# Kernel tuning notes

Measured on AMD Instinct MI355X. Metric: run time of the kernel, lower is better.

## Reference

```python
import jax, jax.numpy as jnp
import numpy as np

EPS = 1e-7
R = 3  # routing iterations


def conv(x, k, b, stride):
    y = jax.lax.conv_general_dilated(x, k, (stride, stride), 'VALID',
                                     dimension_numbers=('NHWC', 'HWIO', 'NHWC'))
    return y + b


def squash(s):
    n = jnp.linalg.norm(s, axis=-1, keepdims=True)
    return (n * n) / (1.0 + n * n) * s / (n + EPS)


def setup_inputs() -> dict:
    key = jax.random.key(0)
    ks = jax.random.split(key, 12)
    B = 256

    def g(k, shape, scale=0.05):
        return jax.random.normal(k, shape, dtype=jnp.float32) * scale

    return dict(
        x=jax.random.normal(ks[0], (B, 40, 40, 1), dtype=jnp.float32),
        y=jax.random.randint(ks[1], (B,), 0, 10),
        conv1_k=g(ks[2], (5, 5, 1, 64)),   conv1_b=jnp.zeros((64,), jnp.float32),
        conv2_k=g(ks[3], (9, 9, 64, 128)), conv2_b=jnp.zeros((128,), jnp.float32),
        conv3_k=g(ks[4], (9, 9, 128, 256)), conv3_b=jnp.zeros((256,), jnp.float32),
        prim_k=g(ks[5], (9, 9, 256, 256)), prim_b=jnp.zeros((256,), jnp.float32),
        w=g(ks[6], (1152, 10, 16, 8)),
        d1_w=g(ks[7], (160, 1024)),  d1_b=jnp.zeros((1024,), jnp.float32),
        d2_w=g(ks[8], (1024, 2048)), d2_b=jnp.zeros((2048,), jnp.float32),
        d3_w=g(ks[9], (2048, 1600)), d3_b=jnp.zeros((1600,), jnp.float32),
    )


def reference(x, y, conv1_k, conv1_b, conv2_k, conv2_b, conv3_k, conv3_b,
              prim_k, prim_b, w, d1_w, d1_b, d2_w, d2_b, d3_w, d3_b):
    # conv stack: 40 -> 36 -> 28 -> 20 -> 6 (primary caps, stride 2, linear)
    h = jax.nn.relu(conv(x, conv1_k, conv1_b, 1))
    h = jax.nn.relu(conv(h, conv2_k, conv2_b, 1))
    h = jax.nn.relu(conv(h, conv3_k, conv3_b, 1))
    h = conv(h, prim_k, prim_b, 2)                      # [B,6,6,256]
    B = h.shape[0]
    u = h.reshape(B, 1152, 8)                           # 1152 primary capsules of dim 8

    # pose predictions: u_hat[b,i,j,k] = sum_v w[i,j,k,v] * u[b,i,v]
    u_hat = jnp.einsum('ijkv,biv->bijk', w, u)          # [B,1152,10,16]

    # dynamic routing by agreement
    b_logit = jnp.zeros((B, 1152, 10), dtype=u_hat.dtype)
    for _ in range(R):
        c = jax.nn.softmax(b_logit, axis=2)[..., None]          # [B,1152,10,1]
        s = jnp.sum(c * u_hat, axis=1, keepdims=True)           # [B,1,10,16]
        v = squash(s)                                           # [B,1,10,16]
        b_logit = b_logit + jnp.sum(u_hat * v, axis=-1)         # agreement

    # masking by true label and reconstruction
    yh = jax.nn.one_hot(y, 10, dtype=v.dtype)                   # [B,10]
    v_masked = yh[:, None, :, None] * v                         # [B,1,10,16]
    v_flat = v_masked.reshape(B, 10 * 16)
    r1 = jax.nn.relu(v_flat @ d1_w + d1_b)
    r2 = jax.nn.relu(r1 @ d2_w + d2_b)
    recon = jax.nn.sigmoid(r2 @ d3_w + d3_b)                    # [B,1600]
    return (v, recon)
```

## Files before the change

kernel.cpp:

```cpp
#include <hip/hip_runtime.h>
#include <hip/hip_bf16.h>

typedef _Float16 f16;
typedef __attribute__((ext_vector_type(8))) _Float16 f16x8;
typedef __attribute__((ext_vector_type(4))) float f32x4;

__device__ __forceinline__ void gload_lds16(const void* g, void* l) {
  __builtin_amdgcn_global_load_lds((const __attribute__((address_space(1))) void*)g,
                                   (__attribute__((address_space(3))) void*)l, 16, 0, 0);
}

template<int CIN, int COUT>
__global__ __launch_bounds__(256) void wtrans_kernel(const float* __restrict__ src,
                                                     f16* __restrict__ dst) {
  constexpr int KT = 81 * CIN;
  __shared__ float tile[64][65];
  int k0 = blockIdx.x * 64;
  int n0 = blockIdx.y * 64;
  int t = threadIdx.x;
#pragma unroll
  for (int i = 0; i < 16; ++i) {
    int id = t + i * 256;
    int r = id >> 6, c = id & 63;
    tile[r][c] = src[(k0 + r) * COUT + n0 + c];
  }
  __syncthreads();
#pragma unroll
  for (int i = 0; i < 16; ++i) {
    int id = t + i * 256;
    int r = id >> 6, c = id & 63;
    dst[(n0 + r) * KT + k0 + c] = (f16)tile[c][r];
  }
}

__global__ __launch_bounds__(256) void wtransg_kernel(const float* __restrict__ src,
                                                      f16* __restrict__ dst,
                                                      int K, int N, int NP) {
  __shared__ float tile[64][65];
  int k0 = blockIdx.x * 64;
  int n0 = blockIdx.y * 64;
  int t = threadIdx.x;
#pragma unroll
  for (int i = 0; i < 16; ++i) {
    int id = t + i * 256;
    int r = id >> 6, c = id & 63;
    tile[r][c] = (n0 + c < N) ? src[(k0 + r) * N + n0 + c] : 0.f;
  }
  __syncthreads();
#pragma unroll
  for (int i = 0; i < 16; ++i) {
    int id = t + i * 256;
    int r = id >> 6, c = id & 63;
    dst[(size_t)(n0 + r) * K + k0 + c] = (f16)tile[c][r];
  }
}

__global__ __launch_bounds__(256) void conv1_kernel(const float* __restrict__ x,
                                                    const float* __restrict__ kw,
                                                    const float* __restrict__ bias,
                                                    f16* __restrict__ out) {
  int idx = blockIdx.x * 256 + threadIdx.x;
  int g = idx & 7;
  int co0 = g * 8;
  int r = idx >> 3;
  int ow = r % 36; int r2 = r / 36; int oh = r2 % 36; int b = r2 / 36;
  float acc[8];
#pragma unroll
  for (int j = 0; j < 8; ++j) acc[j] = bias[co0 + j];
  const float* xp = x + (b * 40 + oh) * 40 + ow;
#pragma unroll
  for (int dy = 0; dy < 5; ++dy)
#pragma unroll
    for (int dx = 0; dx < 5; ++dx) {
      float xv = xp[dy * 40 + dx];
      const float* kp = kw + (dy * 5 + dx) * 64 + co0;
#pragma unroll
      for (int j = 0; j < 8; ++j) acc[j] += xv * kp[j];
    }
  f16x8 o;
#pragma unroll
  for (int j = 0; j < 8; ++j) o[j] = (f16)fmaxf(acc[j], 0.f);
  *(f16x8*)(out + r * 64 + co0) = o;
}

template<int CIN, int WIN>
__device__ __forceinline__ int tapA_off(int kt) {
  int tap, ci0;
  if (CIN == 64)       { tap = kt;      ci0 = 0; }
  else if (CIN == 128) { tap = kt >> 1; ci0 = (kt & 1) << 6; }
  else                 { tap = kt >> 2; ci0 = (kt & 3) << 6; }
  int dy = tap / 9, dx = tap - dy * 9;
  return (dy * WIN + dx) * CIN + ci0;
}

template<int HIN, int WIN, int CIN, int HOUT, int WOUT, int COUT, int STRIDE,
         bool RELU, bool OUTF16>
__global__ __launch_bounds__(512, 2) void conv8p_kernel(const f16* __restrict__ in,
                                                        const f16* __restrict__ wt,
                                                        const float* __restrict__ bias,
                                                        f16* __restrict__ out16,
                                                        float* __restrict__ out32) {
  static_assert(COUT == 256, "BN=256 template requires COUT==256");
  constexpr int KTOT = 81 * CIN;
  constexpr int NT = KTOT / 64;
  __shared__ __align__(16) f16 lds[65536];
  const int mb = (int)blockIdx.x;
  const int t = threadIdx.x;
  const int wave = t >> 6, lane = t & 63;
  const int hi = lane >> 4, lo = lane & 15;
  const int wm = wave >> 2, wn = wave & 3;

  int Aoff[4], Boff[4];
  {
    int g = (lane & 7) ^ ((lane >> 3) & 7);
#pragma unroll
    for (int rbi = 0; rbi < 4; ++rbi) {
      int r = rbi * 64 + 8 * wave + (lane >> 3);
      int m = mb * 256 + r;
      int b = m / (HOUT * WOUT);
      int rr = m - b * (HOUT * WOUT);
      int oh = rr / WOUT, ow = rr - oh * WOUT;
      Aoff[rbi] = ((b * HIN + oh * STRIDE) * WIN + ow * STRIDE) * CIN + g * 8;
      Boff[rbi] = r * KTOT + g * 8;
    }
  }
  const int gb0 = (hi ^ (lo & 7)) << 4;
  const int gb1 = ((4 + hi) ^ (lo & 7)) << 4;

  const char* ldsc = (const char*)lds;
  char* ldsw = (char*)lds;

#define GA(rbi, tpo, bq) gload_lds16(in + Aoff[rbi] + (tpo),                        \
    (void*)(ldsw + (bq) * 32768 + ((rbi) * 64 + 8 * wave) * 128))
#define GB(rbi, tile) gload_lds16(wt + Boff[rbi] + ((tile) << 6),                   \
    (void*)(ldsw + 65536 + ((tile) & 1) * 32768 + ((rbi) * 64 + 8 * wave) * 128))

  {
    int tp0 = tapA_off<CIN, WIN>(0);
    GA(0, tp0, 0); GA(2, tp0, 0); GA(1, tp0, 0); GA(3, tp0, 0);
    GB(0, 0); GB(1, 0); GB(2, 0); GB(3, 0);
    GB(0, 1); GB(1, 1); GB(2, 1); GB(3, 1);
    asm volatile("s_waitcnt vmcnt(4)" ::: "memory");
    __builtin_amdgcn_s_barrier();
  }

  f32x4 acc[8][4] = {};

#define DO_PHASE(Q, STAGE)                                                          \
  {                                                                                 \
    f16x8 af[2][2];                                                                 \
    _Pragma("unroll")                                                               \
    for (int mf = 0; mf < 2; ++mf) {                                                \
      af[mf][0] = *(const f16x8*)(Ab + ((Q) * 2 + mf) * 2048 + gb0);                \
      af[mf][1] = *(const f16x8*)(Ab + ((Q) * 2 + mf) * 2048 + gb1);                \
    }                                                                               \
    STAGE;                                                                          \
    __builtin_amdgcn_s_barrier();                                                   \
    asm volatile("s_waitcnt lgkmcnt(0)" ::: "memory");                              \
    __builtin_amdgcn_sched_barrier(0);                                              \
    __builtin_amdgcn_s_setprio(1);                                                  \
    _Pragma("unroll")                                                               \
    for (int sb = 0; sb < 2; ++sb)                                                  \
      _Pragma("unroll")                                                             \
      for (int mf = 0; mf < 2; ++mf)                                                \
        _Pragma("unroll")                                                           \
        for (int nf = 0; nf < 4; ++nf)                                              \
          acc[(Q) * 2 + mf][nf] = __builtin_amdgcn_mfma_f32_16x16x32_f16(           \
              af[mf][sb], bfr[nf][sb], acc[(Q) * 2 + mf][nf], 0, 0, 0);             \
    __builtin_amdgcn_s_setprio(0);                                                  \
    __builtin_amdgcn_s_barrier();                                                   \
  }

  for (int T = 0; T < NT; ++T) {
    const int q = T & 1;
    const char* Ab = ldsc + q * 32768 + wm * 16384 + lo * 128;
    const char* Bb = ldsc + 65536 + q * 32768 + wn * 8192 + lo * 128;
    const int tpn = tapA_off<CIN, WIN>(T + 1);
    f16x8 bfr[4][2];
#pragma unroll
    for (int nf = 0; nf < 4; ++nf) {
      bfr[nf][0] = *(const f16x8*)(Bb + nf * 2048 + gb0);
      bfr[nf][1] = *(const f16x8*)(Bb + nf * 2048 + gb1);
    }
    DO_PHASE(0, if (T + 1 < NT) { GA(0, tpn, (T + 1) & 1); GA(2, tpn, (T + 1) & 1); })
    DO_PHASE(1, if (T + 1 < NT) { GA(1, tpn, (T + 1) & 1); GA(3, tpn, (T + 1) & 1); })
    DO_PHASE(2, if (T + 2 < NT) { GB(0, T + 2); GB(1, T + 2); })
    DO_PHASE(3,
      if (T + 2 < NT) {
        GB(2, T + 2); GB(3, T + 2);
        asm volatile("s_waitcnt vmcnt(4)" ::: "memory");
      } else {
        asm volatile("s_waitcnt vmcnt(0)" ::: "memory");
      })
  }
#undef DO_PHASE
#undef GA
#undef GB

#pragma unroll
  for (int mfr = 0; mfr < 8; ++mfr) {
#pragma unroll
    for (int nf = 0; nf < 4; ++nf) {
      int m0 = mb * 256 + wm * 128 + mfr * 16 + hi * 4;
      int n = wn * 64 + nf * 16 + lo;
      float bval = bias[n];
#pragma unroll
      for (int r = 0; r < 4; ++r) {
        float v = acc[mfr][nf][r] + bval;
        if (RELU) v = fmaxf(v, 0.f);
        int o = (m0 + r) * COUT + n;
        if (OUTF16) out16[o] = (f16)v; else out32[o] = v;
      }
    }
  }
}

template<int HIN, int WIN, int CIN, int HOUT, int WOUT, int COUT, int STRIDE,
         bool RELU, bool OUTF16, int SPLIT, bool ADDBIAS>
__global__ __launch_bounds__(256) void conv_mfma_kernel(const f16* __restrict__ in,
                                                        const f16* __restrict__ wt,
                                                        const float* __restrict__ bias,
                                                        f16* __restrict__ out16,
                                                        float* __restrict__ out32) {
  constexpr int KTOT = 81 * CIN;
  constexpr int NBLK = COUT / 128;
  constexpr int MTOT = 256 * HOUT * WOUT;
  constexpr int MBNB = (MTOT / 128) * NBLK;
  constexpr int NKT = (KTOT / 64) / SPLIT;
  __shared__ __align__(16) f16 lds[16384];
  int bidx = (int)blockIdx.x;
  int ks = 0;
  if (SPLIT > 1) { ks = bidx / MBNB; bidx -= ks * MBNB; }
  const int mb = bidx / NBLK;
  const int nb = bidx % NBLK;
  const int t = threadIdx.x;
  const int wave = t >> 6, lane = t & 63;
  const int hi = lane >> 4, lo = lane & 15;
  const bool isA = wave < 2;
  const int slot0 = wave << 9;

  int baseoff[8];
#pragma unroll
  for (int it = 0; it < 8; ++it) {
    int s = slot0 + it * 64 + lane;
    if (isA) {
      int row = s >> 3;
      int g = (s & 7) ^ (row & 7);
      int mg = mb * 128 + row;
      int b = mg / (HOUT * WOUT);
      int rr = mg - b * (HOUT * WOUT);
      int oh = rr / WOUT;
      int ow = rr - oh * WOUT;
      baseoff[it] = ((b * HIN + oh * STRIDE) * WIN + ow * STRIDE) * CIN + g * 8;
    } else {
      int sl = s - 1024;
      int row = sl >> 3;
      int g = (sl & 7) ^ (row & 7);
      baseoff[it] = (nb * 128 + row) * KTOT + g * 8;
    }
  }
  const f16* gsrc = isA ? in : wt;

  int aQ[4], bQ[4];
  const int wm = wave >> 1, wn = wave & 1;
#pragma unroll
  for (int f = 0; f < 4; ++f) {
    int arow = wm * 64 + f * 16 + lo;
    aQ[f] = (arow * 128) ^ ((arow & 7) << 4);
    int brow = wn * 64 + f * 16 + lo;
    bQ[f] = 16384 + ((brow * 128) ^ ((brow & 7) << 4));
  }

  f32x4 acc[4][4] = {};
  const char* ldsc = (const char*)lds;

  const int kt0 = ks * NKT;
  for (int kt = kt0; kt < kt0 + NKT; ++kt) {
    int tapoff;
    if (isA) tapoff = tapA_off<CIN, WIN>(kt);
    else     tapoff = kt << 6;
    __syncthreads();
#pragma unroll
    for (int it = 0; it < 8; ++it)
      gload_lds16(gsrc + baseoff[it] + tapoff,
                  (void*)((char*)lds + ((slot0 + it * 64) << 4)));
    __syncthreads();
#pragma unroll
    for (int sub = 0; sub < 2; ++sub) {
      const int gx = (sub * 4 + hi) << 4;
      f16x8 av[4], bv[4];
#pragma unroll
      for (int f = 0; f < 4; ++f) av[f] = *(const f16x8*)(ldsc + (aQ[f] ^ gx));
#pragma unroll
      for (int f = 0; f < 4; ++f) bv[f] = *(const f16x8*)(ldsc + (bQ[f] ^ gx));
#pragma unroll
      for (int mf = 0; mf < 4; ++mf)
#pragma unroll
        for (int nf = 0; nf < 4; ++nf)
          acc[mf][nf] = __builtin_amdgcn_mfma_f32_16x16x32_f16(av[mf], bv[nf],
                                                               acc[mf][nf], 0, 0, 0);
    }
  }

  float* o32 = out32 + (size_t)ks * MTOT * COUT;
#pragma unroll
  for (int mf = 0; mf < 4; ++mf) {
#pragma unroll
    for (int nf = 0; nf < 4; ++nf) {
      int m0 = mb * 128 + wm * 64 + mf * 16 + hi * 4;
      int n = nb * 128 + wn * 64 + nf * 16 + lo;
      float bval = ADDBIAS ? bias[n] : 0.f;
#pragma unroll
      for (int r = 0; r < 4; ++r) {
        float v = acc[mf][nf][r] + bval;
        if (RELU) v = fmaxf(v, 0.f);
        int o = (m0 + r) * COUT + n;
        if (OUTF16) out16[o] = (f16)v; else o32[o] = v;
      }
    }
  }
}

__global__ __launch_bounds__(256) void prim_reduce_kernel(const float* __restrict__ part,
                                                          const float* __restrict__ bias,
                                                          float* __restrict__ p) {
  int idx = blockIdx.x * 256 + threadIdx.x;
  int n = idx & 255;
  float a = bias[n];
#pragma unroll
  for (int s = 0; s < 4; ++s) a += part[s * 2359296 + idx];
  p[idx] = a;
}

template<int K, int NP, int SPLIT>
__global__ __launch_bounds__(256) void gemm_mfma_kernel(const f16* __restrict__ A,
                                                        const f16* __restrict__ Bw,
                                                        float* __restrict__ dpart) {
  constexpr int NBLK = NP / 128;
  constexpr int MBNB = 2 * NBLK;
  constexpr int NKT = (K / 64) / SPLIT;
  __shared__ __align__(16) f16 lds[16384];
  int bidx = (int)blockIdx.x;
  int ks = 0;
  if (SPLIT > 1) { ks = bidx / MBNB; bidx -= ks * MBNB; }
  const int mb = bidx / NBLK;
  const int nb = bidx % NBLK;
  const int t = threadIdx.x;
  const int wave = t >> 6, lane = t & 63;
  const int hi = lane >> 4, lo = lane & 15;
  const bool isA = wave < 2;
  const int slot0 = wave << 9;

  int baseoff[8];
#pragma unroll
  for (int it = 0; it < 8; ++it) {
    int s = slot0 + it * 64 + lane;
    if (isA) {
      int row = s >> 3;
      int g = (s & 7) ^ (row & 7);
      baseoff[it] = (mb * 128 + row) * K + g * 8;
    } else {
      int sl = s - 1024;
      int row = sl >> 3;
      int g = (sl & 7) ^ (row & 7);
      baseoff[it] = (nb * 128 + row) * K + g * 8;
    }
  }
  const f16* gsrc = isA ? A : Bw;

  int aQ[4], bQ[4];
  const int wm = wave >> 1, wn = wave & 1;
#pragma unroll
  for (int f = 0; f < 4; ++f) {
    int arow = wm * 64 + f * 16 + lo;
    aQ[f] = (arow * 128) ^ ((arow & 7) << 4);
    int brow = wn * 64 + f * 16 + lo;
    bQ[f] = 16384 + ((brow * 128) ^ ((brow & 7) << 4));
  }

  f32x4 acc[4][4] = {};
  const char* ldsc = (const char*)lds;

  const int kt0 = ks * NKT;
  for (int kt = kt0; kt < kt0 + NKT; ++kt) {
    int tapoff = kt << 6;
    __syncthreads();
#pragma unroll
    for (int it = 0; it < 8; ++it)
      gload_lds16(gsrc + baseoff[it] + tapoff,
                  (void*)((char*)lds + ((slot0 + it * 64) << 4)));
    __syncthreads();
#pragma unroll
    for (int sub = 0; sub < 2; ++sub) {
      const int gx = (sub * 4 + hi) << 4;
      f16x8 av[4], bv[4];
#pragma unroll
      for (int f = 0; f < 4; ++f) av[f] = *(const f16x8*)(ldsc + (aQ[f] ^ gx));
#pragma unroll
      for (int f = 0; f < 4; ++f) bv[f] = *(const f16x8*)(ldsc + (bQ[f] ^ gx));
#pragma unroll
      for (int mf = 0; mf < 4; ++mf)
#pragma unroll
        for (int nf = 0; nf < 4; ++nf)
          acc[mf][nf] = __builtin_amdgcn_mfma_f32_16x16x32_f16(av[mf], bv[nf],
                                                               acc[mf][nf], 0, 0, 0);
    }
  }

  float* o32 = dpart + (size_t)ks * 256 * NP;
#pragma unroll
  for (int mf = 0; mf < 4; ++mf) {
#pragma unroll
    for (int nf = 0; nf < 4; ++nf) {
      int m0 = mb * 128 + wm * 64 + mf * 16 + hi * 4;
      int n = nb * 128 + wn * 64 + nf * 16 + lo;
#pragma unroll
      for (int r = 0; r < 4; ++r)
        o32[(m0 + r) * NP + n] = acc[mf][nf][r];
    }
  }
}

__global__ __launch_bounds__(256) void d2red_kernel(const float* __restrict__ part,
                                                    const float* __restrict__ bias,
                                                    f16* __restrict__ r2) {
  int idx = blockIdx.x * 256 + threadIdx.x;
  int e0 = idx * 4;
  int n0 = e0 & 2047;
  float4 a = *(const float4*)(part + e0);
  const float4 b1 = *(const float4*)(part + 524288 + e0);
  const float4 b2 = *(const float4*)(part + 1048576 + e0);
  const float4 b3 = *(const float4*)(part + 1572864 + e0);
  float v[4] = {a.x + b1.x + b2.x + b3.x, a.y + b1.y + b2.y + b3.y,
                a.z + b1.z + b2.z + b3.z, a.w + b1.w + b2.w + b3.w};
#pragma unroll
  for (int j = 0; j < 4; ++j)
    r2[e0 + j] = (f16)fmaxf(v[j] + bias[n0 + j], 0.f);
}

__global__ __launch_bounds__(256) void d3red_kernel(const float* __restrict__ part,
                                                    const float* __restrict__ bias,
                                                    float* __restrict__ recon) {
  int idx = blockIdx.x * 256 + threadIdx.x;
  int e0 = idx * 4;
  int n0 = e0 % 1664;
  int m = e0 / 1664;
  float v[4] = {0.f, 0.f, 0.f, 0.f};
#pragma unroll
  for (int s = 0; s < 8; ++s) {
    float4 a = *(const float4*)(part + s * 425984 + e0);
    v[0] += a.x; v[1] += a.y; v[2] += a.z; v[3] += a.w;
  }
#pragma unroll
  for (int j = 0; j < 4; ++j) {
    int n = n0 + j;
    if (n < 1600)
      recon[m * 1600 + n] = 1.f / (1.f + expf(-(v[j] + bias[n])));
  }
}

__global__ __launch_bounds__(320) void uhatps_kernel(const float* __restrict__ wf,
                                                     const float* __restrict__ u,
                                                     f16* __restrict__ uh,
                                                     float* __restrict__ parts) {
  __shared__ float pl[128][8];
  int blk = (int)blockIdx.x;
  int b = blk / 9, ic = blk - b * 9;
  int t = threadIdx.x;
  const float* pb = u + (b * 1152 + ic * 128) * 8;
  for (int e = t; e < 1024; e += 320) pl[e >> 3][e & 7] = pb[e];
  __syncthreads();
  int half = (t >= 160) ? 1 : 0;
  int jk = t - half * 160;
  int ibase = ic * 128 + half * 64;
  float sum = 0.f;
  for (int il = 0; il < 64; ++il) {
    int i = ibase + il;
    const float4* w4 = (const float4*)(wf + (i * 160 + jk) * 8);
    float4 w0 = w4[0], w1 = w4[1];
    const float* pr = pl[half * 64 + il];
    float acc = w0.x * pr[0] + w0.y * pr[1] + w0.z * pr[2] + w0.w * pr[3] +
                w1.x * pr[4] + w1.y * pr[5] + w1.z * pr[6] + w1.w * pr[7];
    uh[(b * 1152 + i) * 160 + jk] = (f16)acc;
    sum += acc;
  }
  parts[(b * 18 + ic * 2 + half) * 160 + jk] = sum;
}

__global__ __launch_bounds__(160) void sred_kernel(const float* __restrict__ parts,
                                                   float cscale, int nch,
                                                   float* __restrict__ vbuf,
                                                   float* __restrict__ vout) {
  int b = blockIdx.x, t = threadIdx.x;
  float s = 0.f;
  for (int c = 0; c < nch; ++c) s += parts[(b * nch + c) * 160 + t];
  s *= cscale;
  float ss = s * s;
  ss += __shfl_xor(ss, 1, 16);
  ss += __shfl_xor(ss, 2, 16);
  ss += __shfl_xor(ss, 4, 16);
  ss += __shfl_xor(ss, 8, 16);
  float n = sqrtf(ss);
  float f = ss / ((1.f + ss) * (n + 1e-7f));
  float v = f * s;
  vbuf[b * 160 + t] = v;
  if (vout) vout[b * 160 + t] = v;
}

template<bool FIRST, bool WRITEB>
__global__ __launch_bounds__(256) void ba_kernel(const f16* __restrict__ uh,
                                                 const float* __restrict__ vbuf,
                                                 float* __restrict__ blog,
                                                 float* __restrict__ parts) {
  __shared__ f16 ul[128 * 172];
  __shared__ float vl[160];
  __shared__ float csm[128 * 10];
  int blk = (int)blockIdx.x;
  int b = blk / 9, ic = blk - b * 9;
  int t = threadIdx.x;
  const f16* ub = uh + (size_t)(b * 1152 + ic * 128) * 160;
  for (int e = t; e < 2560; e += 256) {
    int row = e / 20, col = e - row * 20;
    *(f16x8*)(ul + row * 172 + col * 8) = *(const f16x8*)(ub + row * 160 + col * 8);
  }
  if (t < 160) vl[t] = vbuf[b * 160 + t];
  __syncthreads();

  int il = t >> 1, half = t & 1, j0 = half * 5;
  const f16* ur = ul + il * 172 + j0 * 16;
  float agr[5];
#pragma unroll
  for (int j = 0; j < 5; ++j) {
    f16x8 a0 = *(const f16x8*)(ur + j * 16);
    f16x8 a1 = *(const f16x8*)(ur + j * 16 + 8);
    const float* vv = vl + (j0 + j) * 16;
    float s = (float)a0[0] * vv[0] + (float)a0[1] * vv[1] + (float)a0[2] * vv[2] +
              (float)a0[3] * vv[3] + (float)a0[4] * vv[4] + (float)a0[5] * vv[5] +
              (float)a0[6] * vv[6] + (float)a0[7] * vv[7] +
              (float)a1[0] * vv[8] + (float)a1[1] * vv[9] + (float)a1[2] * vv[10] +
              (float)a1[3] * vv[11] + (float)a1[4] * vv[12] + (float)a1[5] * vv[13] +
              (float)a1[6] * vv[14] + (float)a1[7] * vv[15];
    agr[j] = s;
  }
  int bbase = (b * 1152 + ic * 128 + il) * 10 + j0;
  float bl[5];
#pragma unroll
  for (int j = 0; j < 5; ++j) bl[j] = (FIRST ? 0.f : blog[bbase + j]) + agr[j];
  if (WRITEB) {
#pragma unroll
    for (int j = 0; j < 5; ++j) blog[bbase + j] = bl[j];
  }
  float mx = bl[0];
#pragma unroll
  for (int j = 1; j < 5; ++j) mx = fmaxf(mx, bl[j]);
  mx = fmaxf(mx, __shfl_xor(mx, 1));
  float e5[5], se = 0.f;
#pragma unroll
  for (int j = 0; j < 5; ++j) { e5[j] = expf(bl[j] - mx); se += e5[j]; }
  se += __shfl_xor(se, 1);
  float inv = 1.f / se;
#pragma unroll
  for (int j = 0; j < 5; ++j) csm[il * 10 + j0 + j] = e5[j] * inv;
  __syncthreads();

  if (t < 160) {
    int j = t >> 4;
    float s = 0.f;
    for (int il2 = 0; il2 < 128; ++il2)
      s += csm[il2 * 10 + j] * (float)ul[il2 * 172 + t];
    parts[(b * 9 + ic) * 160 + t] = s;
  }
}

__global__ __launch_bounds__(256) void maskd1_kernel(const float* __restrict__ vbuf,
                                                     const int* __restrict__ y,
                                                     const float* __restrict__ w1,
                                                     const float* __restrict__ b1,
                                                     f16* __restrict__ r1) {
  int idx = blockIdx.x * 256 + threadIdx.x;
  int o = idx & 1023;
  int b = idx >> 10;
  int yb = y[b];
  const float* vv = vbuf + b * 160 + yb * 16;
  float acc = b1[o];
#pragma unroll
  for (int k = 0; k < 16; ++k) acc += vv[k] * w1[(yb * 16 + k) * 1024 + o];
  r1[idx] = (f16)fmaxf(acc, 0.f);
}

extern "C" void kernel_launch(void* const* d_in, const int* in_sizes, int n_in,
                              void* d_out, int out_size, void* d_ws, size_t ws_size,
                              hipStream_t stream) {
  const float* x       = (const float*)d_in[0];
  const int*   y       = (const int*)d_in[1];
  const float* conv1_k = (const float*)d_in[2];
  const float* conv1_b = (const float*)d_in[3];
  const float* conv2_k = (const float*)d_in[4];
  const float* conv2_b = (const float*)d_in[5];
  const float* conv3_k = (const float*)d_in[6];
  const float* conv3_b = (const float*)d_in[7];
  const float* prim_k  = (const float*)d_in[8];
  const float* prim_b  = (const float*)d_in[9];
  const float* w_route = (const float*)d_in[10];
  const float* d1_w = (const float*)d_in[11];
  const float* d1_b = (const float*)d_in[12];
  const float* d2_w = (const float*)d_in[13];
  const float* d2_b = (const float*)d_in[14];
  const float* d3_w = (const float*)d_in[15];
  const float* d3_b = (const float*)d_in[16];

  char* ws = (char*)d_ws;
  f16*   h1     = (f16*)(ws + 0);
  f16*   h2     = (f16*)(ws + 42467328);
  f16*   h3     = (f16*)(ws + 93847552);
  float* part   = (float*)(ws + 0);
  f16*   uhat   = (f16*)(ws + 0);
  float* dpart2 = (float*)(ws + 0);
  float* dpart3 = (float*)(ws + 16777216);
  float* parts  = (float*)(ws + 94371840);
  float* p      = (float*)(ws + 146276352);
  float* blog   = (float*)(ws + 155713536);
  f16*   wd2    = (f16*)(ws + 155713536);
  f16*   wd3    = (f16*)(ws + 159907840);
  float* vbuf   = (float*)(ws + 167510016);
  f16*   r1h    = (f16*)(ws + 167673856);
  f16*   r2h    = (f16*)(ws + 168198144);
  f16*   wt2    = (f16*)(ws + 170819584);
  f16*   wt3    = (f16*)(ws + 172146688);
  f16*   wtp    = (f16*)(ws + 177455104);

  float* vout  = (float*)d_out;
  float* recon = (float*)d_out + 40960;

  wtrans_kernel<64, 128><<<dim3(81, 2), 256, 0, stream>>>(conv2_k, wt2);
  wtrans_kernel<128, 256><<<dim3(162, 4), 256, 0, stream>>>(conv3_k, wt3);
  wtrans_kernel<256, 256><<<dim3(324, 4), 256, 0, stream>>>(prim_k, wtp);

  conv1_kernel<<<10368, 256, 0, stream>>>(x, conv1_k, conv1_b, h1);
  conv_mfma_kernel<36, 36, 64, 28, 28, 128, 1, true, true, 1, true>
      <<<1568, 256, 0, stream>>>(h1, wt2, conv2_b, h2, nullptr);
  conv8p_kernel<28, 28, 128, 20, 20, 256, 1, true, true>
      <<<400, 512, 0, stream>>>(h2, wt3, conv3_b, h3, nullptr);
  conv_mfma_kernel<20, 20, 256, 6, 6, 256, 2, false, false, 4, false>
      <<<576, 256, 0, stream>>>(h3, wtp, prim_b, nullptr, part);
  prim_reduce_kernel<<<9216, 256, 0, stream>>>(part, prim_b, p);

  uhatps_kernel<<<2304, 320, 0, stream>>>(w_route, p, uhat, parts);
  sred_kernel<<<256, 160, 0, stream>>>(parts, 0.1f, 18, vbuf, nullptr);
  ba_kernel<true, true><<<2304, 256, 0, stream>>>(uhat, vbuf, blog, parts);
  sred_kernel<<<256, 160, 0, stream>>>(parts, 1.0f, 9, vbuf, nullptr);
  ba_kernel<false, false><<<2304, 256, 0, stream>>>(uhat, vbuf, blog, parts);
  sred_kernel<<<256, 160, 0, stream>>>(parts, 1.0f, 9, vbuf, vout);

  wtransg_kernel<<<dim3(16, 32), 256, 0, stream>>>(d2_w, wd2, 1024, 2048, 2048);
  wtransg_kernel<<<dim3(32, 26), 256, 0, stream>>>(d3_w, wd3, 2048, 1600, 1664);
  maskd1_kernel<<<1024, 256, 0, stream>>>(vbuf, y, d1_w, d1_b, r1h);
  gemm_mfma_kernel<1024, 2048, 4><<<128, 256, 0, stream>>>(r1h, wd2, dpart2);
  d2red_kernel<<<512, 256, 0, stream>>>(dpart2, d2_b, r2h);
  gemm_mfma_kernel<2048, 1664, 8><<<208, 256, 0, stream>>>(r2h, wd3, dpart3);
  d3red_kernel<<<416, 256, 0, stream>>>(dpart3, d3_b, recon);
}
```

Measured before the change: 1.259 ms.

## Fuse small reduction kernels into consumers and batch weight-transpose launches

Folds the primary-caps split-K reduction into the u_hat kernel and the squash reduction (sred) into each routing kernel and the d1 masking kernel, removing four small launches and their intermediate buffers. The three conv weight transposes and two dense weight transposes are each merged into one launch, and workspace buffers are reassigned with ping-pong routing partials. This cuts launch overhead and global round trips. The cost is that squash is recomputed redundantly in every block (2304 per routing pass) and the workspace aliasing becomes more fragile.

```diff
diff --git a/kernel.cpp b/kernel.cpp
--- a/kernel.cpp
+++ b/kernel.cpp
@@ -10,41 +10,16 @@
                                    (__attribute__((address_space(3))) void*)l, 16, 0, 0);
 }
 
-template<int CIN, int COUT>
-__global__ __launch_bounds__(256) void wtrans_kernel(const float* __restrict__ src,
-                                                     f16* __restrict__ dst) {
-  constexpr int KT = 81 * CIN;
+__device__ __forceinline__ void wtrans_body(const float* __restrict__ src,
+                                            f16* __restrict__ dst,
+                                            int K, int N, int k0, int n0) {
   __shared__ float tile[64][65];
-  int k0 = blockIdx.x * 64;
-  int n0 = blockIdx.y * 64;
   int t = threadIdx.x;
 #pragma unroll
   for (int i = 0; i < 16; ++i) {
     int id = t + i * 256;
     int r = id >> 6, c = id & 63;
-    tile[r][c] = src[(k0 + r) * COUT + n0 + c];
-  }
-  __syncthreads();
-#pragma unroll
-  for (int i = 0; i < 16; ++i) {
-    int id = t + i * 256;
-    int r = id >> 6, c = id & 63;
-    dst[(n0 + r) * KT + k0 + c] = (f16)tile[c][r];
-  }
-}
-
-__global__ __launch_bounds__(256) void wtransg_kernel(const float* __restrict__ src,
-                                                      f16* __restrict__ dst,
-                                                      int K, int N, int NP) {
-  __shared__ float tile[64][65];
-  int k0 = blockIdx.x * 64;
-  int n0 = blockIdx.y * 64;
-  int t = threadIdx.x;
-#pragma unroll
-  for (int i = 0; i < 16; ++i) {
-    int id = t + i * 256;
-    int r = id >> 6, c = id & 63;
-    tile[r][c] = (n0 + c < N) ? src[(k0 + r) * N + n0 + c] : 0.f;
+    tile[r][c] = (n0 + c < N) ? src[(size_t)(k0 + r) * N + n0 + c] : 0.f;
   }
   __syncthreads();
 #pragma unroll
@@ -52,6 +27,34 @@
     int id = t + i * 256;
     int r = id >> 6, c = id & 63;
     dst[(size_t)(n0 + r) * K + k0 + c] = (f16)tile[c][r];
+  }
+}
+
+__global__ __launch_bounds__(256) void wprepc_kernel(const float* __restrict__ s0, f16* __restrict__ d0,
+                                                     const float* __restrict__ s1, f16* __restrict__ d1,
+                                                     const float* __restrict__ s2, f16* __restrict__ d2) {
+  int bid = (int)blockIdx.x;
+  if (bid < 162) {
+    int bx = bid % 81, by = bid / 81;
+    wtrans_body(s0, d0, 5184, 128, bx * 64, by * 64);
+  } else if (bid < 810) {
+    int l = bid - 162; int bx = l % 162, by = l / 162;
+    wtrans_body(s1, d1, 10368, 256, bx * 64, by * 64);
+  } else {
+    int l = bid - 810; int bx = l % 324, by = l / 324;
+    wtrans_body(s2, d2, 20736, 256, bx * 64, by * 64);
+  }
+}
+
+__global__ __launch_bounds__(256) void wprepd_kernel(const float* __restrict__ s0, f16* __restrict__ d0,
+                                                     const float* __restrict__ s1, f16* __restrict__ d1) {
+  int bid = (int)blockIdx.x;
+  if (bid < 512) {
+    int bx = bid % 16, by = bid / 16;
+    wtrans_body(s0, d0, 1024, 2048, bx * 64, by * 64);
+  } else {
+    int l = bid - 512; int bx = l % 32, by = l / 32;
+    wtrans_body(s1, d1, 2048, 1600, bx * 64, by * 64);
   }
 }
 
@@ -321,17 +324,6 @@
   }
 }
 
-__global__ __launch_bounds__(256) void prim_reduce_kernel(const float* __restrict__ part,
-                                                          const float* __restrict__ bias,
-                                                          float* __restrict__ p) {
-  int idx = blockIdx.x * 256 + threadIdx.x;
-  int n = idx & 255;
-  float a = bias[n];
-#pragma unroll
-  for (int s = 0; s < 4; ++s) a += part[s * 2359296 + idx];
-  p[idx] = a;
-}
-
 template<int K, int NP, int SPLIT>
 __global__ __launch_bounds__(256) void gemm_mfma_kernel(const f16* __restrict__ A,
                                                         const f16* __restrict__ Bw,
@@ -460,15 +452,21 @@
 }
 
 __global__ __launch_bounds__(320) void uhatps_kernel(const float* __restrict__ wf,
-                                                     const float* __restrict__ u,
+                                                     const float* __restrict__ part,
+                                                     const float* __restrict__ pbias,
                                                      f16* __restrict__ uh,
                                                      float* __restrict__ parts) {
   __shared__ float pl[128][8];
   int blk = (int)blockIdx.x;
   int b = blk / 9, ic = blk - b * 9;
   int t = threadIdx.x;
-  const float* pb = u + (b * 1152 + ic * 128) * 8;
-  for (int e = t; e < 1024; e += 320) pl[e >> 3][e & 7] = pb[e];
+  const int base = b * 9216 + ic * 1024;
+  for (int e = t; e < 1024; e += 320) {
+    float a = pbias[e & 255];
+#pragma unroll
+    for (int s = 0; s < 4; ++s) a += part[s * 2359296 + base + e];
+    pl[e >> 3][e & 7] = a;
+  }
   __syncthreads();
   int half = (t >= 160) ? 1 : 0;
   int jk = t - half * 160;
@@ -487,31 +485,12 @@
   parts[(b * 18 + ic * 2 + half) * 160 + jk] = sum;
 }
 
-__global__ __launch_bounds__(160) void sred_kernel(const float* __restrict__ parts,
-                                                   float cscale, int nch,
-                                                   float* __restrict__ vbuf,
-                                                   float* __restrict__ vout) {
-  int b = blockIdx.x, t = threadIdx.x;
-  float s = 0.f;
-  for (int c = 0; c < nch; ++c) s += parts[(b * nch + c) * 160 + t];
-  s *= cscale;
-  float ss = s * s;
-  ss += __shfl_xor(ss, 1, 16);
-  ss += __shfl_xor(ss, 2, 16);
-  ss += __shfl_xor(ss, 4, 16);
-  ss += __shfl_xor(ss, 8, 16);
-  float n = sqrtf(ss);
-  float f = ss / ((1.f + ss) * (n + 1e-7f));
-  float v = f * s;
-  vbuf[b * 160 + t] = v;
-  if (vout) vout[b * 160 + t] = v;
-}
-
-template<bool FIRST, bool WRITEB>
+template<int NCH, bool FIRST, bool WRITEB>
 __global__ __launch_bounds__(256) void ba_kernel(const f16* __restrict__ uh,
-                                                 const float* __restrict__ vbuf,
+                                                 const float* __restrict__ psrc,
+                                                 float cscale,
                                                  float* __restrict__ blog,
-                                                 float* __restrict__ parts) {
+                                                 float* __restrict__ pdst) {
   __shared__ f16 ul[128 * 172];
   __shared__ float vl[160];
   __shared__ float csm[128 * 10];
@@ -523,7 +502,19 @@
     int row = e / 20, col = e - row * 20;
     *(f16x8*)(ul + row * 172 + col * 8) = *(const f16x8*)(ub + row * 160 + col * 8);
   }
-  if (t < 160) vl[t] = vbuf[b * 160 + t];
+  if (t < 160) {
+    float s = 0.f;
+    for (int c = 0; c < NCH; ++c) s += psrc[(b * NCH + c) * 160 + t];
+    s *= cscale;
+    float ss = s * s;
+    ss += __shfl_xor(ss, 1, 16);
+    ss += __shfl_xor(ss, 2, 16);
+    ss += __shfl_xor(ss, 4, 16);
+    ss += __shfl_xor(ss, 8, 16);
+    float n = sqrtf(ss);
+    float f = ss / ((1.f + ss) * (n + 1e-7f));
+    vl[t] = f * s;
+  }
   __syncthreads();
 
   int il = t >> 1, half = t & 1, j0 = half * 5;
@@ -568,24 +559,38 @@
     float s = 0.f;
     for (int il2 = 0; il2 < 128; ++il2)
       s += csm[il2 * 10 + j] * (float)ul[il2 * 172 + t];
-    parts[(b * 9 + ic) * 160 + t] = s;
-  }
-}
-
-__global__ __launch_bounds__(256) void maskd1_kernel(const float* __restrict__ vbuf,
-                                                     const int* __restrict__ y,
-                                                     const float* __restrict__ w1,
-                                                     const float* __restrict__ b1,
-                                                     f16* __restrict__ r1) {
-  int idx = blockIdx.x * 256 + threadIdx.x;
-  int o = idx & 1023;
-  int b = idx >> 10;
+    pdst[(b * 9 + ic) * 160 + t] = s;
+  }
+}
+
+__global__ __launch_bounds__(1024) void maskd1v_kernel(const float* __restrict__ parts,
+                                                       const int* __restrict__ y,
+                                                       const float* __restrict__ w1,
+                                                       const float* __restrict__ b1,
+                                                       float* __restrict__ vout,
+                                                       f16* __restrict__ r1) {
+  __shared__ float vl[160];
+  int b = blockIdx.x, t = threadIdx.x;
+  if (t < 160) {
+    float s = 0.f;
+    for (int c = 0; c < 9; ++c) s += parts[(b * 9 + c) * 160 + t];
+    float ss = s * s;
+    ss += __shfl_xor(ss, 1, 16);
+    ss += __shfl_xor(ss, 2, 16);
+    ss += __shfl_xor(ss, 4, 16);
+    ss += __shfl_xor(ss, 8, 16);
+    float n = sqrtf(ss);
+    float f = ss / ((1.f + ss) * (n + 1e-7f));
+    float v = f * s;
+    vl[t] = v;
+    vout[b * 160 + t] = v;
+  }
+  __syncthreads();
   int yb = y[b];
-  const float* vv = vbuf + b * 160 + yb * 16;
-  float acc = b1[o];
-#pragma unroll
-  for (int k = 0; k < 16; ++k) acc += vv[k] * w1[(yb * 16 + k) * 1024 + o];
-  r1[idx] = (f16)fmaxf(acc, 0.f);
+  float acc = b1[t];
+#pragma unroll
+  for (int k = 0; k < 16; ++k) acc += vl[yb * 16 + k] * w1[(yb * 16 + k) * 1024 + t];
+  r1[b * 1024 + t] = (f16)fmaxf(acc, 0.f);
 }
 
 extern "C" void kernel_launch(void* const* d_in, const int* in_sizes, int n_in,
@@ -610,31 +615,28 @@
   const float* d3_b = (const float*)d_in[16];
 
   char* ws = (char*)d_ws;
-  f16*   h1     = (f16*)(ws + 0);
-  f16*   h2     = (f16*)(ws + 42467328);
-  f16*   h3     = (f16*)(ws + 93847552);
-  float* part   = (float*)(ws + 0);
-  f16*   uhat   = (f16*)(ws + 0);
-  float* dpart2 = (float*)(ws + 0);
-  float* dpart3 = (float*)(ws + 16777216);
-  float* parts  = (float*)(ws + 94371840);
-  float* p      = (float*)(ws + 146276352);
-  float* blog   = (float*)(ws + 155713536);
-  f16*   wd2    = (f16*)(ws + 155713536);
-  f16*   wd3    = (f16*)(ws + 159907840);
-  float* vbuf   = (float*)(ws + 167510016);
-  f16*   r1h    = (f16*)(ws + 167673856);
-  f16*   r2h    = (f16*)(ws + 168198144);
-  f16*   wt2    = (f16*)(ws + 170819584);
-  f16*   wt3    = (f16*)(ws + 172146688);
-  f16*   wtp    = (f16*)(ws + 177455104);
+  f16*   h1      = (f16*)(ws + 0);
+  float* part    = (float*)(ws + 0);
+  float* dpart2  = (float*)(ws + 0);
+  float* dpart3  = (float*)(ws + 16777216);
+  f16*   h2      = (f16*)(ws + 42467328);
+  f16*   uhat    = (f16*)(ws + 42467328);
+  f16*   h3      = (f16*)(ws + 93847552);
+  float* parts_a = (float*)(ws + 146276352);
+  float* parts_b = (float*)(ws + 149225472);
+  float* blog    = (float*)(ws + 155713536);
+  f16*   r1h     = (f16*)(ws + 167673856);
+  f16*   r2h     = (f16*)(ws + 168198144);
+  f16*   wt2     = (f16*)(ws + 170819584);
+  f16*   wt3     = (f16*)(ws + 172146688);
+  f16*   wtp     = (f16*)(ws + 177455104);
+  f16*   wd2     = (f16*)(ws + 177455104);
+  f16*   wd3     = (f16*)(ws + 181649408);
 
   float* vout  = (float*)d_out;
   float* recon = (float*)d_out + 40960;
 
-  wtrans_kernel<64, 128><<<dim3(81, 2), 256, 0, stream>>>(conv2_k, wt2);
-  wtrans_kernel<128, 256><<<dim3(162, 4), 256, 0, stream>>>(conv3_k, wt3);
-  wtrans_kernel<256, 256><<<dim3(324, 4), 256, 0, stream>>>(prim_k, wtp);
+  wprepc_kernel<<<2106, 256, 0, stream>>>(conv2_k, wt2, conv3_k, wt3, prim_k, wtp);
 
   conv1_kernel<<<10368, 256, 0, stream>>>(x, conv1_k, conv1_b, h1);
   conv_mfma_kernel<36, 36, 64, 28, 28, 128, 1, true, true, 1, true>
@@ -643,18 +645,13 @@
       <<<400, 512, 0, stream>>>(h2, wt3, conv3_b, h3, nullptr);
   conv_mfma_kernel<20, 20, 256, 6, 6, 256, 2, false, false, 4, false>
       <<<576, 256, 0, stream>>>(h3, wtp, prim_b, nullptr, part);
-  prim_reduce_kernel<<<9216, 256, 0, stream>>>(part, prim_b, p);
-
-  uhatps_kernel<<<2304, 320, 0, stream>>>(w_route, p, uhat, parts);
-  sred_kernel<<<256, 160, 0, stream>>>(parts, 0.1f, 18, vbuf, nullptr);
-  ba_kernel<true, true><<<2304, 256, 0, stream>>>(uhat, vbuf, blog, parts);
-  sred_kernel<<<256, 160, 0, stream>>>(parts, 1.0f, 9, vbuf, nullptr);
-  ba_kernel<false, false><<<2304, 256, 0, stream>>>(uhat, vbuf, blog, parts);
-  sred_kernel<<<256, 160, 0, stream>>>(parts, 1.0f, 9, vbuf, vout);
-
-  wtransg_kernel<<<dim3(16, 32), 256, 0, stream>>>(d2_w, wd2, 1024, 2048, 2048);
-  wtransg_kernel<<<dim3(32, 26), 256, 0, stream>>>(d3_w, wd3, 2048, 1600, 1664);
-  maskd1_kernel<<<1024, 256, 0, stream>>>(vbuf, y, d1_w, d1_b, r1h);
+
+  uhatps_kernel<<<2304, 320, 0, stream>>>(w_route, part, prim_b, uhat, parts_a);
+  wprepd_kernel<<<1344, 256, 0, stream>>>(d2_w, wd2, d3_w, wd3);
+  ba_kernel<18, true, true><<<2304, 256, 0, stream>>>(uhat, parts_a, 0.1f, blog, parts_b);
+  ba_kernel<9, false, false><<<2304, 256, 0, stream>>>(uhat, parts_b, 1.0f, blog, parts_a);
+
+  maskd1v_kernel<<<256, 1024, 0, stream>>>(parts_a, y, d1_w, d1_b, vout, r1h);
   gemm_mfma_kernel<1024, 2048, 4><<<128, 256, 0, stream>>>(r1h, wd2, dpart2);
   d2red_kernel<<<512, 256, 0, stream>>>(dpart2, d2_b, r2h);
   gemm_mfma_kernel<2048, 1664, 8><<<208, 256, 0, stream>>>(r2h, wd3, dpart3);
```

New measurement: 1.226 ms. 2.7% less time.
